# Kernel tuning notes

Hardware: AMD Instinct MI355X
Metric: run time of the kernel (lower is better)

Reference implementation:

```python
import jax, jax.numpy as jnp
import numpy as np

B, T, D = 256, 128, 64
H, A, O = 512, 128, 32


def setup_inputs() -> dict:
    key = jax.random.key(0)
    ks = jax.random.split(key, 16)
    u = lambda k, sh, lo, hi: jax.random.uniform(k, sh, jnp.float32, lo, hi)
    return {
        "x_states": jax.random.normal(ks[0], (B, T, D), jnp.float32),
        "x_dts": jax.random.uniform(ks[1], (B, T), jnp.float32) * 0.1,
        # StepwiseAttention params (stored [in, out])
        "Wq": u(ks[2], (D, A), -0.1, 0.1), "bq": u(ks[3], (A,), -0.1, 0.1),
        "Wk": u(ks[4], (H, A), -0.1, 0.1), "bk": u(ks[5], (A,), -0.1, 0.1),
        "Wv": u(ks[6], (H, A), -0.1, 0.1), "bv": u(ks[7], (A,), -0.1, 0.1),
        # LTCAttentionCell params
        "W_gd": u(ks[8], (D + H + A, 2 * H), -0.1, 0.1),
        "b_gd": u(ks[9], (2 * H,), -0.1, 0.1),
        "W_tau": u(ks[10], (H, H), -0.1, 0.1),
        "b_tau": u(ks[11], (H,), -0.1, 0.1),
        "gleak": u(ks[12], (H,), 0.001, 1.0),
        "cm": u(ks[13], (H,), 0.4, 0.6),
        # output head
        "W_fc": u(ks[14], (H, O), -0.1, 0.1),
        "b_fc": u(ks[15], (O,), -0.1, 0.1),
    }


def _forward(x_states, x_dts, Wq, bq, Wk, bk, Wv, bv,
             W_gd, b_gd, W_tau, b_tau, gleak, cm, W_fc, b_fc):
    scale = jnp.sqrt(jnp.asarray(A, jnp.float32))
    leak = jax.nn.softplus(cm) + jax.nn.softplus(gleak)  # [H]

    def dhdt(h, x_t, ctx):
        combined = jnp.concatenate([x_t, h, ctx], axis=1)        # [B, D+H+A]
        gd = combined @ W_gd + b_gd                              # [B, 2H]
        gate, dyn = jnp.split(gd, 2, axis=1)
        tau = jax.nn.softplus(h @ W_tau + b_tau)                 # [B, H]
        num = jax.nn.sigmoid(gate) * jnp.tanh(dyn) - h
        return num / (tau + leak + 1e-6)

    def step(carry, inp):
        h, hist = carry            # h [B,H], hist [B,T,H]
        t, x_t, dt = inp           # t scalar, x_t [B,D], dt [B]
        # stepwise attention over history h_1..h_t
        Q = x_t @ Wq + bq                                        # [B, A]
        K = hist @ Wk + bk                                       # [B, T, A]
        V = hist @ Wv + bv                                       # [B, T, A]
        scores = jnp.einsum('ba,bta->bt', Q, K) / scale          # [B, T]
        valid = jnp.arange(T) < t
        scores = jnp.where(valid[None, :], scores, -1e9)
        w = jax.nn.softmax(scores, axis=-1)
        ctx = jnp.einsum('bt,bta->ba', w, V)
        ctx = jnp.where(t > 0, ctx, jnp.zeros_like(ctx))         # empty history -> 0
        # one RK4 step (torchdiffeq 'rk4' = 3/8-rule variant), step size dt per sample
        dtc = dt[:, None]
        k1 = dhdt(h, x_t, ctx)
        k2 = dhdt(h + dtc * k1 / 3.0, x_t, ctx)
        k3 = dhdt(h + dtc * (k2 - k1 / 3.0), x_t, ctx)
        k4 = dhdt(h + dtc * (k1 - k2 + k3), x_t, ctx)
        h_next = h + dtc * (k1 + 3.0 * k2 + 3.0 * k3 + k4) / 8.0
        hist = jax.lax.dynamic_update_slice(hist, h_next[:, None, :], (0, t, 0))
        return (h_next, hist), None

    h0 = jnp.zeros((B, H), jnp.float32)
    hist0 = jnp.zeros((B, T, H), jnp.float32)
    xs = (jnp.arange(T), jnp.swapaxes(x_states, 0, 1), jnp.swapaxes(x_dts, 0, 1))
    (h_final, _), _ = jax.lax.scan(step, (h0, hist0), xs)
    return h_final @ W_fc + b_fc                                 # [B, O]


def reference(x_states, x_dts, Wq, bq, Wk, bk, Wv, bv,
              W_gd, b_gd, W_tau, b_tau, gleak, cm, W_fc, b_fc):
    return _forward(x_states, x_dts, Wq, bq, Wk, bk, Wv, bv,
                    W_gd, b_gd, W_tau, b_tau, gleak, cm, W_fc, b_fc)
```

## Files before the change

kernel.cpp:

```cpp
#include <hip/hip_runtime.h>
#include <math.h>

#define B_ 256
#define T_ 128
#define D_ 64
#define H_ 512
#define A_ 128
#define O_ 32

typedef __attribute__((ext_vector_type(8))) short short8;
typedef __attribute__((ext_vector_type(8))) unsigned short ushort8;
typedef __attribute__((ext_vector_type(4))) float floatx4;
typedef __attribute__((ext_vector_type(4))) unsigned int uintx4;
typedef unsigned long long ull;

__device__ __forceinline__ float sp_(float x) {
    return fmaxf(x, 0.f) + log1pf(expf(-fabsf(x)));
}
__device__ __forceinline__ float sigm_(float x) {
    return 1.f / (1.f + expf(-x));
}
__device__ __forceinline__ unsigned short f2bf_(float f) {
    unsigned int u = __float_as_uint(f);
    return (unsigned short)((u + 0x7FFFu + ((u >> 16) & 1u)) >> 16);
}
__device__ __forceinline__ float bf2f_(unsigned short u) {
    return __uint_as_float(((unsigned)u) << 16);
}

__device__ __forceinline__ void ld16sc(uintx4& d, const void* p) {
    asm volatile("global_load_dwordx4 %0, %1, off sc0 sc1"
                 : "=v"(d) : "v"(p) : "memory");
}
__device__ __forceinline__ void ld4sc(float& d, const void* p) {
    asm volatile("global_load_dword %0, %1, off sc0 sc1"
                 : "=v"(d) : "v"(p) : "memory");
}
__device__ __forceinline__ void ld4su(unsigned& d, const void* p) {
    asm volatile("global_load_dword %0, %1, off sc0 sc1"
                 : "=v"(d) : "v"(p) : "memory");
}
__device__ __forceinline__ void st64sc(ull* p, ull v) {
    asm volatile("global_store_dwordx2 %0, %1, off sc0 sc1"
                 :: "v"(p), "v"(v) : "memory");
}
__device__ __forceinline__ void stu32sc(unsigned* p, unsigned v) {
    asm volatile("global_store_dword %0, %1, off sc0 sc1"
                 :: "v"(p), "v"(v) : "memory");
}
__device__ __forceinline__ void vmwait4(uintx4& a, uintx4& b, uintx4& c,
                                        uintx4& d) {
    asm volatile("s_waitcnt vmcnt(0)"
                 : "+v"(a), "+v"(b), "+v"(c), "+v"(d)::"memory");
}
__device__ __forceinline__ void vmwait8(uintx4& a, uintx4& b, uintx4& c,
                                        uintx4& d, uintx4& e, uintx4& f,
                                        uintx4& g, uintx4& h) {
    asm volatile("s_waitcnt vmcnt(0)"
                 : "+v"(a), "+v"(b), "+v"(c), "+v"(d), "+v"(e), "+v"(f),
                   "+v"(g), "+v"(h)::"memory");
}
__device__ __forceinline__ void vmwait16f(float& a0, float& a1, float& a2,
                                          float& a3, float& a4, float& a5,
                                          float& a6, float& a7, float& b0,
                                          float& b1, float& b2, float& b3,
                                          float& b4, float& b5, float& b6,
                                          float& b7) {
    asm volatile("s_waitcnt vmcnt(0)"
                 : "+v"(a0), "+v"(a1), "+v"(a2), "+v"(a3), "+v"(a4), "+v"(a5),
                   "+v"(a6), "+v"(a7), "+v"(b0), "+v"(b1), "+v"(b2), "+v"(b3),
                   "+v"(b4), "+v"(b5), "+v"(b6), "+v"(b7)::"memory");
}
__device__ __forceinline__ void vmwait8u(unsigned& a, unsigned& b, unsigned& c,
                                         unsigned& d, unsigned& e, unsigned& f,
                                         unsigned& g, unsigned& h) {
    asm volatile("s_waitcnt vmcnt(0)"
                 : "+v"(a), "+v"(b), "+v"(c), "+v"(d), "+v"(e), "+v"(f),
                   "+v"(g), "+v"(h)::"memory");
}
__device__ __forceinline__ void vmwait4u(unsigned& a, unsigned& b, unsigned& c,
                                         unsigned& d) {
    asm volatile("s_waitcnt vmcnt(0)"
                 : "+v"(a), "+v"(b), "+v"(c), "+v"(d)::"memory");
}
__device__ __forceinline__ void vmwait1u(unsigned& a) {
    asm volatile("s_waitcnt vmcnt(0)" : "+v"(a)::"memory");
}
__device__ __forceinline__ floatx4 u2f_(uintx4 u) {
    union { uintx4 u; floatx4 f; } c;
    c.u = u;
    return c.f;
}
__device__ __forceinline__ void stf_(float* p, float v) {
    __hip_atomic_store(p, v, __ATOMIC_RELAXED, __HIP_MEMORY_SCOPE_SYSTEM);
}

__global__ void init_kernel(unsigned short* __restrict__ hpack,
                            unsigned* __restrict__ bar) {
    int i = blockIdx.x * 256 + threadIdx.x;
    if (i < B_ * H_) hpack[i] = 0;
    if (i < 18432) bar[i] = 0u;
}

__global__ void pack_w_kernel(const float* __restrict__ W_gd,
                              const float* __restrict__ W_tau,
                              const float* __restrict__ Wk,
                              const float* __restrict__ Wv,
                              unsigned short* __restrict__ Wpack) {
    int gid = blockIdx.x * 256 + threadIdx.x;
    if (gid >= 1114112) return;
    int j = gid & 7;
    int l = (gid >> 3) & 63;
    int kpart = (l >> 4) * 8 + j;
    int npart = l & 15;
    float v;
    if (gid < 786432) {
        int f = gid >> 9;
        int s = f % 3;
        int rem = f / 3;
        int kb = rem & 15, ct = rem >> 4;
        int k = kb * 32 + kpart;
        int c = ct * 16 + npart;
        if (s == 0)      v = W_gd[(size_t)(D_ + k) * 1024 + c];
        else if (s == 1) v = W_gd[(size_t)(D_ + k) * 1024 + 512 + c];
        else             v = W_tau[(size_t)k * 512 + c];
    } else if (gid < 851968) {
        int r = gid - 786432;
        int f = r >> 9;
        int s = f & 1, kb = (f >> 1) & 1, ct = f >> 2;
        int k = kb * 32 + kpart;
        int c = ct * 16 + npart;
        v = W_gd[(size_t)k * 1024 + s * 512 + c];
    } else if (gid < 983040) {
        int r = gid - 851968;
        int f = r >> 9;
        int s = f & 1, kb = (f >> 1) & 3, ct = f >> 3;
        int k = kb * 32 + kpart;
        int c = ct * 16 + npart;
        v = W_gd[(size_t)(D_ + H_ + k) * 1024 + s * 512 + c];
    } else {
        int r = gid - 983040;
        int f = r >> 9;
        int kb = f & 15, c4 = f >> 4;
        int k = kb * 32 + kpart;
        int n = (c4 & 7) * 16 + npart;
        v = (c4 < 8) ? Wk[(size_t)k * A_ + n] : Wv[(size_t)k * A_ + n];
    }
    Wpack[gid] = f2bf_(v);
}

__device__ __forceinline__ void gsyncF(unsigned* flags, int j, unsigned cnt) {
    asm volatile("s_waitcnt vmcnt(0)" ::: "memory");
    __syncthreads();
    if (threadIdx.x == 0) stu32sc(flags + j * 64, cnt);
    if (threadIdx.x < 8) {
        unsigned v;
        do {
            ld4su(v, flags + threadIdx.x * 64);
            vmwait1u(v);
            if (v >= cnt) break;
            __builtin_amdgcn_s_sleep(1);
        } while (true);
    }
    __syncthreads();
}

struct P {
    const float *x, *dts, *Wq, *bq, *bk, *bv, *b_gd, *b_tau, *gleak, *cm,
        *W_fc, *b_fc;
    float *h, *ctx, *out, *Kpart, *Vpart;
    unsigned short* Kh;
    const unsigned short *Wy, *Wx, *Wc, *Wkv;
    unsigned short *hpack, *yapack, *ybpack, *ycpack;
    unsigned* bar;
};

__global__ __launch_bounds__(256, 1) void fused_kernel(P p) {
    const int tid = threadIdx.x;
    const int bid = blockIdx.x;
    const int lane = tid & 63;
    const int wave = tid >> 6;
    const int g = bid & 15;
    const int j = bid >> 4;
    const int ct = j * 4 + wave;
    unsigned* flags = p.bar + g * 512;
    unsigned* senbase = p.bar + 8192;
    #define SEN(kind, src) (senbase + (((kind)*16 + g) * 8 + (src)) * 16)

    __shared__ float WqL[D_ * 129];
    __shared__ float xs4[2][D_];
    __shared__ float q4[2][A_];
    __shared__ float sc4[2][T_];
    __shared__ float red[2][2];
    __shared__ __align__(16) unsigned short AsL[32 * 256];
    __shared__ __align__(16) unsigned short ypbuf[4 * 256];
    __shared__ __align__(16) unsigned short As2[2 * 512];
    __shared__ unsigned short VhL[2][A_][136];

    const int quad = lane >> 4;
    const int c = ct * 16 + (lane & 15);
    const float btau = p.b_tau[c];
    const float lk = sp_(p.cm[c]) + sp_(p.gleak[c]) + 1e-6f;
    const float bgd_g = p.b_gd[c];
    const float bgd_d = p.b_gd[512 + c];
    const int aoff = (quad >> 1) * 256 + (lane & 15) * 16 + (quad & 1) * 8;
    const int ypw = wave * 256 + (lane & 15);

    const int sub = tid >> 7;
    const int tl = tid & 127;
    const int r = g * 16 + j * 2 + sub;
    const int rrow = r & 15;

    short8 wg[16], wd[16], wt[16];
    short8 wxg[2], wxd[2], wcg[4], wcd[4];
    {
        const short8* Wy8 = (const short8*)p.Wy;
        #pragma unroll
        for (int kb = 0; kb < 16; ++kb) {
            wg[kb] = Wy8[((ct * 16 + kb) * 3 + 0) * 64 + lane];
            wd[kb] = Wy8[((ct * 16 + kb) * 3 + 1) * 64 + lane];
            wt[kb] = Wy8[((ct * 16 + kb) * 3 + 2) * 64 + lane];
        }
        const short8* Wx8 = (const short8*)p.Wx;
        const short8* Wc8 = (const short8*)p.Wc;
        #pragma unroll
        for (int kb = 0; kb < 2; ++kb) {
            wxg[kb] = Wx8[((ct * 2 + kb) * 2 + 0) * 64 + lane];
            wxd[kb] = Wx8[((ct * 2 + kb) * 2 + 1) * 64 + lane];
        }
        #pragma unroll
        for (int kb = 0; kb < 4; ++kb) {
            wcg[kb] = Wc8[((ct * 4 + kb) * 2 + 0) * 64 + lane];
            wcd[kb] = Wc8[((ct * 4 + kb) * 2 + 1) * 64 + lane];
        }
    }

    for (int i = tid; i < D_ * A_; i += 256) {
        int d = i >> 7, a = i & 127;
        WqL[d * 129 + a] = p.Wq[i];
    }

    floatx4 hreg = {0.f, 0.f, 0.f, 0.f};
    floatx4 rk1, rk2, rk3, baseg, based, ycur, dt4;

    const short8* Wkv8 = (const short8*)p.Wkv;

    __syncthreads();

    for (int t = 0; t < T_; ++t) {
        {
            float kk[8], vv[8];
            uintx4 av[4];
            {
                const unsigned short* src = p.hpack + g * 8192;
                const unsigned expv = (unsigned)t;
                unsigned s0, s1, s2, s3, s4, s5, s6, s7;
                for (;;) {
                    #pragma unroll
                    for (int jj = 0; jj < 8; ++jj) {
                        ld4sc(kk[jj],
                              p.Kpart + ((g * 8 + jj) * 16 + rrow) * 128 + tl);
                        ld4sc(vv[jj],
                              p.Vpart + ((g * 8 + jj) * 16 + rrow) * 128 + tl);
                    }
                    #pragma unroll
                    for (int i = 0; i < 4; ++i)
                        ld16sc(av[i], src + (size_t)tid * 8 + i * 2048);
                    ld4su(s0, SEN(4, 0)); ld4su(s1, SEN(4, 1));
                    ld4su(s2, SEN(4, 2)); ld4su(s3, SEN(4, 3));
                    ld4su(s4, SEN(4, 4)); ld4su(s5, SEN(4, 5));
                    ld4su(s6, SEN(4, 6)); ld4su(s7, SEN(4, 7));
                    vmwait16f(kk[0], kk[1], kk[2], kk[3], kk[4], kk[5], kk[6],
                              kk[7], vv[0], vv[1], vv[2], vv[3], vv[4], vv[5],
                              vv[6], vv[7]);
                    vmwait4(av[0], av[1], av[2], av[3]);
                    vmwait8u(s0, s1, s2, s3, s4, s5, s6, s7);
                    if (s0 >= expv && s1 >= expv && s2 >= expv && s3 >= expv &&
                        s4 >= expv && s5 >= expv && s6 >= expv && s7 >= expv)
                        break;
                    __builtin_amdgcn_s_sleep(1);
                }
            }
            #pragma unroll
            for (int i = 0; i < 4; ++i)
                ((uintx4*)AsL)[tid + i * 256] = av[i];
            if (t > 0) {
                float ks = p.bk[tl], vs = p.bv[tl];
                #pragma unroll
                for (int jj = 0; jj < 8; ++jj) {
                    ks += kk[jj];
                    vs += vv[jj];
                }
                p.Kh[(size_t)(r * T_ + (t - 1)) * A_ + tl] = f2bf_(ks);
                VhL[sub][tl][t - 1] = f2bf_(vs);
            }
            if (tl < 16)
                ((float4*)xs4[sub])[tl] =
                    ((const float4*)&p.x[(r * T_ + t) * D_])[tl];
            __syncthreads();
            float qa = p.bq[tl];
            #pragma unroll 8
            for (int d = 0; d < D_; ++d) qa += xs4[sub][d] * WqL[d * 129 + tl];
            q4[sub][tl] = qa;
            __syncthreads();
            if (t == 0) {
                stf_(p.ctx + r * A_ + tl, 0.f);
            } else {
                const float rscale = 0.08838834764831845f;
                const int grp = tl >> 4, ln = tl & 15;
                float qv[8];
                #pragma unroll
                for (int i = 0; i < 8; ++i) qv[i] = q4[sub][ln * 8 + i];
                for (int s = grp; s < t; s += 8) {
                    ushort8 k8 = *((const ushort8*)(p.Kh +
                                     (size_t)(r * T_ + s) * A_) + ln);
                    float a2 = 0.f;
                    #pragma unroll
                    for (int i = 0; i < 8; ++i) a2 += bf2f_(k8[i]) * qv[i];
                    #pragma unroll
                    for (int off = 8; off > 0; off >>= 1)
                        a2 += __shfl_xor(a2, off, 16);
                    if (ln == 0) sc4[sub][s] = a2 * rscale;
                }
                __syncthreads();
                float mloc = -1e30f;
                for (int s = tl; s < t; s += 128) mloc = fmaxf(mloc, sc4[sub][s]);
                #pragma unroll
                for (int off = 32; off > 0; off >>= 1)
                    mloc = fmaxf(mloc, __shfl_xor(mloc, off, 64));
                if (lane == 0) red[sub][wave & 1] = mloc;
                __syncthreads();
                float m = fmaxf(red[sub][0], red[sub][1]);
                float ssum = 0.f;
                for (int s = tl; s < t; s += 128) {
                    float e = expf(sc4[sub][s] - m);
                    sc4[sub][s] = e;
                    ssum += e;
                }
                #pragma unroll
                for (int off = 32; off > 0; off >>= 1)
                    ssum += __shfl_xor(ssum, off, 64);
                __syncthreads();
                if (lane == 0) red[sub][wave & 1] = ssum;
                __syncthreads();
                float rs = 1.f / (red[sub][0] + red[sub][1]);
                const unsigned short* Vrow = &VhL[sub][tl][0];
                float ca0 = 0.f, ca1 = 0.f;
                int s0 = 0;
                for (; s0 + 16 <= t; s0 += 16) {
                    ushort8 v0 = *(const ushort8*)(Vrow + s0);
                    ushort8 v1 = *(const ushort8*)(Vrow + s0 + 8);
                    #pragma unroll
                    for (int i = 0; i < 8; ++i) {
                        ca0 += sc4[sub][s0 + i] * bf2f_(v0[i]);
                        ca1 += sc4[sub][s0 + 8 + i] * bf2f_(v1[i]);
                    }
                }
                if (s0 + 8 <= t) {
                    ushort8 v0 = *(const ushort8*)(Vrow + s0);
                    #pragma unroll
                    for (int i = 0; i < 8; ++i)
                        ca0 += sc4[sub][s0 + i] * bf2f_(v0[i]);
                    s0 += 8;
                }
                for (; s0 < t; ++s0) ca0 += sc4[sub][s0] * bf2f_(Vrow[s0]);
                stf_(p.ctx + r * A_ + tl, (ca0 + ca1) * rs);
            }
        }
        asm volatile("s_waitcnt vmcnt(0)" ::: "memory");
        __syncthreads();
        if (tid == 0) stu32sc(SEN(0, j), (unsigned)(t + 1));

        {
            const int mrow = lane & 15;
            const float* crow = &p.ctx[(g * 16 + mrow) * A_];
            uintx4 cc[8];
            {
                const unsigned* senp = SEN(0, mrow >> 1);
                const unsigned expv = (unsigned)(t + 1);
                unsigned sv;
                for (;;) {
                    #pragma unroll
                    for (int kb = 0; kb < 4; ++kb) {
                        ld16sc(cc[2 * kb], crow + kb * 32 + quad * 8);
                        ld16sc(cc[2 * kb + 1], crow + kb * 32 + quad * 8 + 4);
                    }
                    ld4su(sv, senp);
                    vmwait8(cc[0], cc[1], cc[2], cc[3], cc[4], cc[5], cc[6],
                            cc[7]);
                    vmwait1u(sv);
                    if (sv >= expv) break;
                    __builtin_amdgcn_s_sleep(1);
                }
            }
            #pragma unroll
            for (int i = 0; i < 4; ++i)
                dt4[i] = p.dts[(g * 16 + quad * 4 + i) * T_ + t];

            floatx4 bg = {0.f, 0.f, 0.f, 0.f};
            floatx4 bd = {0.f, 0.f, 0.f, 0.f};
            const float4* xrow =
                (const float4*)&p.x[((g * 16 + mrow) * T_ + t) * D_];
            #pragma unroll
            for (int kb = 0; kb < 2; ++kb) {
                float4 u = xrow[kb * 8 + quad * 2], v = xrow[kb * 8 + quad * 2 + 1];
                short8 ax;
                ax[0] = (short)f2bf_(u.x); ax[1] = (short)f2bf_(u.y);
                ax[2] = (short)f2bf_(u.z); ax[3] = (short)f2bf_(u.w);
                ax[4] = (short)f2bf_(v.x); ax[5] = (short)f2bf_(v.y);
                ax[6] = (short)f2bf_(v.z); ax[7] = (short)f2bf_(v.w);
                bg = __builtin_amdgcn_mfma_f32_16x16x32_bf16(ax, wxg[kb], bg, 0, 0, 0);
                bd = __builtin_amdgcn_mfma_f32_16x16x32_bf16(ax, wxd[kb], bd, 0, 0, 0);
            }
            #pragma unroll
            for (int kb = 0; kb < 4; ++kb) {
                floatx4 f0 = u2f_(cc[2 * kb]), f1 = u2f_(cc[2 * kb + 1]);
                short8 ac;
                ac[0] = (short)f2bf_(f0[0]); ac[1] = (short)f2bf_(f0[1]);
                ac[2] = (short)f2bf_(f0[2]); ac[3] = (short)f2bf_(f0[3]);
                ac[4] = (short)f2bf_(f1[0]); ac[5] = (short)f2bf_(f1[1]);
                ac[6] = (short)f2bf_(f1[2]); ac[7] = (short)f2bf_(f1[3]);
                bg = __builtin_amdgcn_mfma_f32_16x16x32_bf16(ac, wcg[kb], bg, 0, 0, 0);
                bd = __builtin_amdgcn_mfma_f32_16x16x32_bf16(ac, wcd[kb], bd, 0, 0, 0);
            }
            floatx4 ag = {0.f, 0.f, 0.f, 0.f};
            floatx4 ad = {0.f, 0.f, 0.f, 0.f};
            floatx4 at = {0.f, 0.f, 0.f, 0.f};
            #pragma unroll
            for (int kb = 0; kb < 16; ++kb) {
                short8 a = *(const short8*)(AsL + kb * 512 + aoff);
                ag = __builtin_amdgcn_mfma_f32_16x16x32_bf16(a, wg[kb], ag, 0, 0, 0);
                ad = __builtin_amdgcn_mfma_f32_16x16x32_bf16(a, wd[kb], ad, 0, 0, 0);
                at = __builtin_amdgcn_mfma_f32_16x16x32_bf16(a, wt[kb], at, 0, 0, 0);
            }
            #pragma unroll
            for (int i = 0; i < 4; ++i) {
                baseg[i] = bg[i] + bgd_g;
                based[i] = bd[i] + bgd_d;
                float gate = ag[i] + baseg[i];
                float dyn = ad[i] + based[i];
                float tau = sp_(at[i] + btau);
                float ki = (sigm_(gate) * tanhf(dyn) - hreg[i]) / (tau + lk);
                rk1[i] = ki;
                float yn = hreg[i] + dt4[i] * ki * (1.f / 3.f);
                ycur[i] = yn;
                ypbuf[ypw + (quad * 4 + i) * 16] = f2bf_(yn);
            }
            __syncthreads();
            st64sc((ull*)p.yapack + g * 2048 + j * 256 + tid,
                   ((const ull*)ypbuf)[tid]);
        }
        asm volatile("s_waitcnt vmcnt(0)" ::: "memory");
        __syncthreads();
        if (tid == 0) stu32sc(SEN(1, j), (unsigned)(t + 1));

        #pragma unroll 1
        for (int stage = 2; stage <= 4; ++stage) {
            const unsigned short* ysrc =
                (stage == 2) ? p.yapack : (stage == 3) ? p.ybpack : p.ycpack;
            unsigned short* ydst =
                (stage == 2) ? p.ybpack : (stage == 3) ? p.ycpack : p.hpack;
            const int senk = stage - 1;
            {
                const unsigned short* src = ysrc + g * 8192;
                const unsigned expv = (unsigned)(t + 1);
                const int sb = tid >> 7;
                uintx4 av[4];
                unsigned s0, s1, s2, s3;
                for (;;) {
                    #pragma unroll
                    for (int i = 0; i < 4; ++i)
                        ld16sc(av[i], src + (size_t)tid * 8 + i * 2048);
                    ld4su(s0, SEN(senk, sb + 0));
                    ld4su(s1, SEN(senk, sb + 2));
                    ld4su(s2, SEN(senk, sb + 4));
                    ld4su(s3, SEN(senk, sb + 6));
                    vmwait4(av[0], av[1], av[2], av[3]);
                    vmwait4u(s0, s1, s2, s3);
                    if (s0 >= expv && s1 >= expv && s2 >= expv && s3 >= expv)
                        break;
                    __builtin_amdgcn_s_sleep(1);
                }
                #pragma unroll
                for (int i = 0; i < 4; ++i)
                    ((uintx4*)AsL)[tid + i * 256] = av[i];
            }
            __syncthreads();
            floatx4 ag = {0.f, 0.f, 0.f, 0.f};
            floatx4 ad = {0.f, 0.f, 0.f, 0.f};
            floatx4 at = {0.f, 0.f, 0.f, 0.f};
            #pragma unroll
            for (int kb = 0; kb < 16; ++kb) {
                short8 a = *(const short8*)(AsL + kb * 512 + aoff);
                ag = __builtin_amdgcn_mfma_f32_16x16x32_bf16(a, wg[kb], ag, 0, 0, 0);
                ad = __builtin_amdgcn_mfma_f32_16x16x32_bf16(a, wd[kb], ad, 0, 0, 0);
                at = __builtin_amdgcn_mfma_f32_16x16x32_bf16(a, wt[kb], at, 0, 0, 0);
            }
            const int lane_p = ((c >> 3) & 3) * 16;
            #pragma unroll
            for (int i = 0; i < 4; ++i) {
                float gate = ag[i] + baseg[i];
                float dyn = ad[i] + based[i];
                float tau = sp_(at[i] + btau);
                float ki = (sigm_(gate) * tanhf(dyn) - ycur[i]) / (tau + lk);
                float yn;
                if (stage == 2) {
                    rk2[i] = ki;
                    yn = hreg[i] + dt4[i] * (ki - rk1[i] * (1.f / 3.f));
                } else if (stage == 3) {
                    rk3[i] = ki;
                    yn = hreg[i] + dt4[i] * (rk1[i] - rk2[i] + ki);
                } else {
                    yn = hreg[i] +
                         dt4[i] * (rk1[i] + 3.f * rk2[i] + 3.f * rk3[i] + ki) * 0.125f;
                    hreg[i] = yn;
                }
                ycur[i] = yn;
                ypbuf[ypw + (quad * 4 + i) * 16] = f2bf_(yn);
                if (stage == 4)
                    As2[(wave >> 1) * 512 + (c & 7) +
                        (lane_p + quad * 4 + i) * 8] = f2bf_(yn);
            }
            __syncthreads();
            st64sc((ull*)ydst + g * 2048 + j * 256 + tid,
                   ((const ull*)ypbuf)[tid]);
            if (stage == 4) {
                #pragma unroll
                for (int h4 = 0; h4 < 4; ++h4) {
                    const int c4 = wave + h4 * 4;
                    floatx4 acc = {0.f, 0.f, 0.f, 0.f};
                    #pragma unroll
                    for (int kk2 = 0; kk2 < 2; ++kk2) {
                        short8 a = *(const short8*)(As2 + (kk2 * 64 + lane) * 8);
                        acc = __builtin_amdgcn_mfma_f32_16x16x32_bf16(
                            a, Wkv8[(c4 * 16 + (j * 2 + kk2)) * 64 + lane], acc,
                            0, 0, 0);
                    }
                    const int ac = (c4 & 7) * 16 + (lane & 15);
                    float* part = (c4 < 8) ? p.Kpart : p.Vpart;
                    #pragma unroll
                    for (int i = 0; i < 4; ++i)
                        stf_(part + ((g * 8 + j) * 16 + quad * 4 + i) * 128 + ac,
                             acc[i]);
                }
            }
            asm volatile("s_waitcnt vmcnt(0)" ::: "memory");
            __syncthreads();
            if (tid == 0) stu32sc(SEN(stage, j), (unsigned)(t + 1));
        }
    }

    #pragma unroll
    for (int i = 0; i < 4; ++i)
        stf_(p.h + (g * 16 + quad * 4 + i) * H_ + c, hreg[i]);
    gsyncF(flags, j, 1u);
    {
        const int o = tl & 31, ks = tl >> 5;
        float acc = 0.f;
        const float* hrow = p.h + r * H_ + ks * 128;
        const float* wcol = p.W_fc + ks * 128 * O_ + o;
        #pragma unroll 1
        for (int rd = 0; rd < 4; ++rd) {
            uintx4 hh[8];
            #pragma unroll
            for (int i = 0; i < 8; ++i)
                ld16sc(hh[i], hrow + rd * 32 + i * 4);
            vmwait8(hh[0], hh[1], hh[2], hh[3], hh[4], hh[5], hh[6], hh[7]);
            #pragma unroll
            for (int i = 0; i < 8; ++i) {
                floatx4 f = u2f_(hh[i]);
                #pragma unroll
                for (int e = 0; e < 4; ++e)
                    acc += f[e] * wcol[(rd * 32 + i * 4 + e) * O_];
            }
        }
        sc4[sub][tl] = acc;
        __syncthreads();
        if (ks == 0)
            p.out[r * O_ + o] = acc + sc4[sub][o + 32] + sc4[sub][o + 64] +
                                sc4[sub][o + 96] + p.b_fc[o];
    }
    #undef SEN
}

extern "C" void kernel_launch(void* const* d_in, const int* in_sizes, int n_in,
                              void* d_out, int out_size, void* d_ws,
                              size_t ws_size, hipStream_t stream) {
    (void)in_sizes; (void)n_in; (void)out_size; (void)ws_size;
    P p;
    p.x = (const float*)d_in[0];
    p.dts = (const float*)d_in[1];
    p.Wq = (const float*)d_in[2];
    p.bq = (const float*)d_in[3];
    const float* Wk = (const float*)d_in[4];
    p.bk = (const float*)d_in[5];
    const float* Wv = (const float*)d_in[6];
    p.bv = (const float*)d_in[7];
    const float* W_gd = (const float*)d_in[8];
    p.b_gd = (const float*)d_in[9];
    const float* W_tau = (const float*)d_in[10];
    p.b_tau = (const float*)d_in[11];
    p.gleak = (const float*)d_in[12];
    p.cm = (const float*)d_in[13];
    p.W_fc = (const float*)d_in[14];
    p.b_fc = (const float*)d_in[15];
    p.out = (float*)d_out;

    float* ws = (float*)d_ws;
    p.h = ws;
    p.ctx = p.h + B_ * H_;
    p.Kpart = p.ctx + B_ * A_;
    p.Vpart = p.Kpart + 262144;
    unsigned short* Wpack = (unsigned short*)(p.Vpart + 262144);
    p.Wy = Wpack;
    p.Wx = Wpack + 786432;
    p.Wc = Wpack + 851968;
    p.Wkv = Wpack + 983040;
    p.hpack = Wpack + 1114112;
    p.yapack = p.hpack + B_ * H_;
    p.ybpack = p.yapack + B_ * H_;
    p.ycpack = p.ybpack + B_ * H_;
    p.Kh = p.ycpack + B_ * H_;
    p.bar = (unsigned*)(p.Kh + (size_t)B_ * T_ * A_);

    init_kernel<<<512, 256, 0, stream>>>(p.hpack, p.bar);
    pack_w_kernel<<<4352, 256, 0, stream>>>(W_gd, W_tau, Wk, Wv, Wpack);

    fused_kernel<<<dim3(128), dim3(256), 0, stream>>>(p);
}
```

Baseline: 3.529 ms.

## Precompute partial attention over older history during stage 4, merge newest entry online

The attention over history h_1..h_{t-1} for step t+1 is now computed right after stage 4 of step t, using known keys, and stored as unnormalized numerator, denominator and max. At the start of the next step only the newest key/value row (K/V projection of h_t via MFMA over the full hidden vector) is computed locally and merged with an online-softmax update. This removes the separate ctx barrier/flag and the Kpart/Vpart cross-block reduction from the critical path. In exchange each block redoes the full 512-wide K/V projection for 16 rows and adds more LDS buffers.

```diff
diff --git a/kernel.cpp b/kernel.cpp
--- a/kernel.cpp
+++ b/kernel.cpp
@@ -32,10 +32,6 @@
     asm volatile("global_load_dwordx4 %0, %1, off sc0 sc1"
                  : "=v"(d) : "v"(p) : "memory");
 }
-__device__ __forceinline__ void ld4sc(float& d, const void* p) {
-    asm volatile("global_load_dword %0, %1, off sc0 sc1"
-                 : "=v"(d) : "v"(p) : "memory");
-}
 __device__ __forceinline__ void ld4su(unsigned& d, const void* p) {
     asm volatile("global_load_dword %0, %1, off sc0 sc1"
                  : "=v"(d) : "v"(p) : "memory");
@@ -60,16 +56,9 @@
                  : "+v"(a), "+v"(b), "+v"(c), "+v"(d), "+v"(e), "+v"(f),
                    "+v"(g), "+v"(h)::"memory");
 }
-__device__ __forceinline__ void vmwait16f(float& a0, float& a1, float& a2,
-                                          float& a3, float& a4, float& a5,
-                                          float& a6, float& a7, float& b0,
-                                          float& b1, float& b2, float& b3,
-                                          float& b4, float& b5, float& b6,
-                                          float& b7) {
+__device__ __forceinline__ void vmwait3c(uintx4& a, uintx4& b, uintx4& c) {
     asm volatile("s_waitcnt vmcnt(0)"
-                 : "+v"(a0), "+v"(a1), "+v"(a2), "+v"(a3), "+v"(a4), "+v"(a5),
-                   "+v"(a6), "+v"(a7), "+v"(b0), "+v"(b1), "+v"(b2), "+v"(b3),
-                   "+v"(b4), "+v"(b5), "+v"(b6), "+v"(b7)::"memory");
+                 : "+v"(a), "+v"(b), "+v"(c)::"memory");
 }
 __device__ __forceinline__ void vmwait8u(unsigned& a, unsigned& b, unsigned& c,
                                          unsigned& d, unsigned& e, unsigned& f,
@@ -168,7 +157,7 @@
 struct P {
     const float *x, *dts, *Wq, *bq, *bk, *bv, *b_gd, *b_tau, *gleak, *cm,
         *W_fc, *b_fc;
-    float *h, *ctx, *out, *Kpart, *Vpart;
+    float *h, *ctxB, *out;
     unsigned short* Kh;
     const unsigned short *Wy, *Wx, *Wc, *Wkv;
     unsigned short *hpack, *yapack, *ybpack, *ycpack;
@@ -194,8 +183,10 @@
     __shared__ float red[2][2];
     __shared__ __align__(16) unsigned short AsL[32 * 256];
     __shared__ __align__(16) unsigned short ypbuf[4 * 256];
-    __shared__ __align__(16) unsigned short As2[2 * 512];
     __shared__ unsigned short VhL[2][A_][136];
+    __shared__ __align__(16) float xsLf[16][68];
+    __shared__ __align__(16) unsigned short KVt[2][16][136];
+    __shared__ __align__(16) float ctxL[16][132];
 
     const int quad = lane >> 4;
     const int c = ct * 16 + (lane & 15);
@@ -209,7 +200,9 @@
     const int sub = tid >> 7;
     const int tl = tid & 127;
     const int r = g * 16 + j * 2 + sub;
-    const int rrow = r & 15;
+    const int row16 = tid >> 4;
+    const int k16 = tid & 15;
+    const float rscale = 0.08838834764831845f;
 
     short8 wg[16], wd[16], wt[16];
     short8 wxg[2], wxd[2], wcg[4], wcd[4];
@@ -248,155 +241,114 @@
     __syncthreads();
 
     for (int t = 0; t < T_; ++t) {
+        uintx4 cb0 = {0, 0, 0, 0}, cb1 = {0, 0, 0, 0}, cbs = {0, 0, 0, 0};
         {
-            float kk[8], vv[8];
             uintx4 av[4];
-            {
-                const unsigned short* src = p.hpack + g * 8192;
-                const unsigned expv = (unsigned)t;
-                unsigned s0, s1, s2, s3, s4, s5, s6, s7;
-                for (;;) {
-                    #pragma unroll
-                    for (int jj = 0; jj < 8; ++jj) {
-                        ld4sc(kk[jj],
-                              p.Kpart + ((g * 8 + jj) * 16 + rrow) * 128 + tl);
-                        ld4sc(vv[jj],
-                              p.Vpart + ((g * 8 + jj) * 16 + rrow) * 128 + tl);
-                    }
-                    #pragma unroll
-                    for (int i = 0; i < 4; ++i)
-                        ld16sc(av[i], src + (size_t)tid * 8 + i * 2048);
-                    ld4su(s0, SEN(4, 0)); ld4su(s1, SEN(4, 1));
-                    ld4su(s2, SEN(4, 2)); ld4su(s3, SEN(4, 3));
-                    ld4su(s4, SEN(4, 4)); ld4su(s5, SEN(4, 5));
-                    ld4su(s6, SEN(4, 6)); ld4su(s7, SEN(4, 7));
-                    vmwait16f(kk[0], kk[1], kk[2], kk[3], kk[4], kk[5], kk[6],
-                              kk[7], vv[0], vv[1], vv[2], vv[3], vv[4], vv[5],
-                              vv[6], vv[7]);
-                    vmwait4(av[0], av[1], av[2], av[3]);
-                    vmwait8u(s0, s1, s2, s3, s4, s5, s6, s7);
-                    if (s0 >= expv && s1 >= expv && s2 >= expv && s3 >= expv &&
-                        s4 >= expv && s5 >= expv && s6 >= expv && s7 >= expv)
-                        break;
-                    __builtin_amdgcn_s_sleep(1);
+            const unsigned short* srcp = p.hpack + g * 8192;
+            const float* cbrow = p.ctxB + (size_t)(g * 16 + row16) * 132;
+            const unsigned expv = (unsigned)t;
+            unsigned s0, s1, s2, s3, s4, s5, s6, s7;
+            for (;;) {
+                #pragma unroll
+                for (int i = 0; i < 4; ++i)
+                    ld16sc(av[i], srcp + (size_t)tid * 8 + i * 2048);
+                if (t > 0) {
+                    ld16sc(cb0, cbrow + k16 * 8);
+                    ld16sc(cb1, cbrow + k16 * 8 + 4);
+                    ld16sc(cbs, cbrow + 128);
                 }
+                ld4su(s0, SEN(4, 0)); ld4su(s1, SEN(4, 1));
+                ld4su(s2, SEN(4, 2)); ld4su(s3, SEN(4, 3));
+                ld4su(s4, SEN(4, 4)); ld4su(s5, SEN(4, 5));
+                ld4su(s6, SEN(4, 6)); ld4su(s7, SEN(4, 7));
+                vmwait4(av[0], av[1], av[2], av[3]);
+                if (t > 0) vmwait3c(cb0, cb1, cbs);
+                vmwait8u(s0, s1, s2, s3, s4, s5, s6, s7);
+                if (s0 >= expv && s1 >= expv && s2 >= expv && s3 >= expv &&
+                    s4 >= expv && s5 >= expv && s6 >= expv && s7 >= expv)
+                    break;
+                __builtin_amdgcn_s_sleep(1);
             }
             #pragma unroll
             for (int i = 0; i < 4; ++i)
                 ((uintx4*)AsL)[tid + i * 256] = av[i];
-            if (t > 0) {
-                float ks = p.bk[tl], vs = p.bv[tl];
-                #pragma unroll
-                for (int jj = 0; jj < 8; ++jj) {
-                    ks += kk[jj];
-                    vs += vv[jj];
+            if (t > 0 && tid < 64)
+                ((float4*)&xsLf[tid >> 2][0])[tid & 3] =
+                    ((const float4*)&p.x[((g * 16 + (tid >> 2)) * T_ + t) *
+                                         D_])[tid & 3];
+        }
+        __syncthreads();
+
+        if (t > 0) {
+            #pragma unroll
+            for (int h4 = 0; h4 < 4; ++h4) {
+                const int c4 = wave + h4 * 4;
+                floatx4 acc = {0.f, 0.f, 0.f, 0.f};
+                #pragma unroll
+                for (int kb = 0; kb < 16; ++kb) {
+                    short8 a = *(const short8*)(AsL + kb * 512 + aoff);
+                    acc = __builtin_amdgcn_mfma_f32_16x16x32_bf16(
+                        a, Wkv8[(c4 * 16 + kb) * 64 + lane], acc, 0, 0, 0);
                 }
-                p.Kh[(size_t)(r * T_ + (t - 1)) * A_ + tl] = f2bf_(ks);
-                VhL[sub][tl][t - 1] = f2bf_(vs);
-            }
-            if (tl < 16)
-                ((float4*)xs4[sub])[tl] =
-                    ((const float4*)&p.x[(r * T_ + t) * D_])[tl];
+                const int ac = (c4 & 7) * 16 + (lane & 15);
+                const float bias = ((c4 < 8) ? p.bk : p.bv)[ac];
+                #pragma unroll
+                for (int i = 0; i < 4; ++i)
+                    KVt[c4 >= 8 ? 1 : 0][quad * 4 + i][ac] =
+                        f2bf_(acc[i] + bias);
+            }
             __syncthreads();
-            float qa = p.bq[tl];
-            #pragma unroll 8
-            for (int d = 0; d < D_; ++d) qa += xs4[sub][d] * WqL[d * 129 + tl];
-            q4[sub][tl] = qa;
+            {
+                float qa[8];
+                #pragma unroll
+                for (int n = 0; n < 8; ++n) qa[n] = p.bq[k16 * 8 + n];
+                for (int d = 0; d < D_; ++d) {
+                    float xv = xsLf[row16][d];
+                    #pragma unroll
+                    for (int n = 0; n < 8; ++n)
+                        qa[n] += xv * WqL[d * 129 + k16 * 8 + n];
+                }
+                ushort8 k8 = *(const ushort8*)&KVt[0][row16][k16 * 8];
+                float sm = 0.f;
+                #pragma unroll
+                for (int n = 0; n < 8; ++n) sm += qa[n] * bf2f_(k8[n]);
+                #pragma unroll
+                for (int off = 8; off > 0; off >>= 1)
+                    sm += __shfl_xor(sm, off, 16);
+                sm *= rscale;
+                floatx4 cbf = u2f_(cbs);
+                const float denb = cbf[0], mb = cbf[1];
+                const float m = fmaxf(mb, sm);
+                const float wb = expf(mb - m), wm = expf(sm - m);
+                const float rs = 1.f / (denb * wb + wm);
+                floatx4 n0 = u2f_(cb0), n1 = u2f_(cb1);
+                ushort8 v8 = *(const ushort8*)&KVt[1][row16][k16 * 8];
+                #pragma unroll
+                for (int n = 0; n < 4; ++n)
+                    ctxL[row16][k16 * 8 + n] =
+                        (n0[n] * wb + wm * bf2f_(v8[n])) * rs;
+                #pragma unroll
+                for (int n = 0; n < 4; ++n)
+                    ctxL[row16][k16 * 8 + 4 + n] =
+                        (n1[n] * wb + wm * bf2f_(v8[4 + n])) * rs;
+            }
             __syncthreads();
-            if (t == 0) {
-                stf_(p.ctx + r * A_ + tl, 0.f);
-            } else {
-                const float rscale = 0.08838834764831845f;
-                const int grp = tl >> 4, ln = tl & 15;
-                float qv[8];
-                #pragma unroll
-                for (int i = 0; i < 8; ++i) qv[i] = q4[sub][ln * 8 + i];
-                for (int s = grp; s < t; s += 8) {
-                    ushort8 k8 = *((const ushort8*)(p.Kh +
-                                     (size_t)(r * T_ + s) * A_) + ln);
-                    float a2 = 0.f;
-                    #pragma unroll
-                    for (int i = 0; i < 8; ++i) a2 += bf2f_(k8[i]) * qv[i];
-                    #pragma unroll
-                    for (int off = 8; off > 0; off >>= 1)
-                        a2 += __shfl_xor(a2, off, 16);
-                    if (ln == 0) sc4[sub][s] = a2 * rscale;
-                }
-                __syncthreads();
-                float mloc = -1e30f;
-                for (int s = tl; s < t; s += 128) mloc = fmaxf(mloc, sc4[sub][s]);
-                #pragma unroll
-                for (int off = 32; off > 0; off >>= 1)
-                    mloc = fmaxf(mloc, __shfl_xor(mloc, off, 64));
-                if (lane == 0) red[sub][wave & 1] = mloc;
-                __syncthreads();
-                float m = fmaxf(red[sub][0], red[sub][1]);
-                float ssum = 0.f;
-                for (int s = tl; s < t; s += 128) {
-                    float e = expf(sc4[sub][s] - m);
-                    sc4[sub][s] = e;
-                    ssum += e;
-                }
-                #pragma unroll
-                for (int off = 32; off > 0; off >>= 1)
-                    ssum += __shfl_xor(ssum, off, 64);
-                __syncthreads();
-                if (lane == 0) red[sub][wave & 1] = ssum;
-                __syncthreads();
-                float rs = 1.f / (red[sub][0] + red[sub][1]);
-                const unsigned short* Vrow = &VhL[sub][tl][0];
-                float ca0 = 0.f, ca1 = 0.f;
-                int s0 = 0;
-                for (; s0 + 16 <= t; s0 += 16) {
-                    ushort8 v0 = *(const ushort8*)(Vrow + s0);
-                    ushort8 v1 = *(const ushort8*)(Vrow + s0 + 8);
-                    #pragma unroll
-                    for (int i = 0; i < 8; ++i) {
-                        ca0 += sc4[sub][s0 + i] * bf2f_(v0[i]);
-                        ca1 += sc4[sub][s0 + 8 + i] * bf2f_(v1[i]);
-                    }
-                }
-                if (s0 + 8 <= t) {
-                    ushort8 v0 = *(const ushort8*)(Vrow + s0);
-                    #pragma unroll
-                    for (int i = 0; i < 8; ++i)
-                        ca0 += sc4[sub][s0 + i] * bf2f_(v0[i]);
-                    s0 += 8;
-                }
-                for (; s0 < t; ++s0) ca0 += sc4[sub][s0] * bf2f_(Vrow[s0]);
-                stf_(p.ctx + r * A_ + tl, (ca0 + ca1) * rs);
-            }
-        }
-        asm volatile("s_waitcnt vmcnt(0)" ::: "memory");
-        __syncthreads();
-        if (tid == 0) stu32sc(SEN(0, j), (unsigned)(t + 1));
+            {
+                const int rl = j * 2 + sub;
+                p.Kh[(size_t)(r * T_ + (t - 1)) * A_ + tl] = KVt[0][rl][tl];
+                VhL[sub][tl][t - 1] = KVt[1][rl][tl];
+            }
+        } else {
+            #pragma unroll
+            for (int n = 0; n < 8; ++n) ctxL[row16][k16 * 8 + n] = 0.f;
+            __syncthreads();
+        }
 
         {
-            const int mrow = lane & 15;
-            const float* crow = &p.ctx[(g * 16 + mrow) * A_];
-            uintx4 cc[8];
-            {
-                const unsigned* senp = SEN(0, mrow >> 1);
-                const unsigned expv = (unsigned)(t + 1);
-                unsigned sv;
-                for (;;) {
-                    #pragma unroll
-                    for (int kb = 0; kb < 4; ++kb) {
-                        ld16sc(cc[2 * kb], crow + kb * 32 + quad * 8);
-                        ld16sc(cc[2 * kb + 1], crow + kb * 32 + quad * 8 + 4);
-                    }
-                    ld4su(sv, senp);
-                    vmwait8(cc[0], cc[1], cc[2], cc[3], cc[4], cc[5], cc[6],
-                            cc[7]);
-                    vmwait1u(sv);
-                    if (sv >= expv) break;
-                    __builtin_amdgcn_s_sleep(1);
-                }
-            }
             #pragma unroll
             for (int i = 0; i < 4; ++i)
                 dt4[i] = p.dts[(g * 16 + quad * 4 + i) * T_ + t];
-
+            const int mrow = lane & 15;
             floatx4 bg = {0.f, 0.f, 0.f, 0.f};
             floatx4 bd = {0.f, 0.f, 0.f, 0.f};
             const float4* xrow =
@@ -414,12 +366,13 @@
             }
             #pragma unroll
             for (int kb = 0; kb < 4; ++kb) {
-                floatx4 f0 = u2f_(cc[2 * kb]), f1 = u2f_(cc[2 * kb + 1]);
+                float4 f0 = *(const float4*)&ctxL[mrow][kb * 32 + quad * 8];
+                float4 f1 = *(const float4*)&ctxL[mrow][kb * 32 + quad * 8 + 4];
                 short8 ac;
-                ac[0] = (short)f2bf_(f0[0]); ac[1] = (short)f2bf_(f0[1]);
-                ac[2] = (short)f2bf_(f0[2]); ac[3] = (short)f2bf_(f0[3]);
-                ac[4] = (short)f2bf_(f1[0]); ac[5] = (short)f2bf_(f1[1]);
-                ac[6] = (short)f2bf_(f1[2]); ac[7] = (short)f2bf_(f1[3]);
+                ac[0] = (short)f2bf_(f0.x); ac[1] = (short)f2bf_(f0.y);
+                ac[2] = (short)f2bf_(f0.z); ac[3] = (short)f2bf_(f0.w);
+                ac[4] = (short)f2bf_(f1.x); ac[5] = (short)f2bf_(f1.y);
+                ac[6] = (short)f2bf_(f1.z); ac[7] = (short)f2bf_(f1.w);
                 bg = __builtin_amdgcn_mfma_f32_16x16x32_bf16(ac, wcg[kb], bg, 0, 0, 0);
                 bd = __builtin_amdgcn_mfma_f32_16x16x32_bf16(ac, wcd[kb], bd, 0, 0, 0);
             }
@@ -496,7 +449,6 @@
                 ad = __builtin_amdgcn_mfma_f32_16x16x32_bf16(a, wd[kb], ad, 0, 0, 0);
                 at = __builtin_amdgcn_mfma_f32_16x16x32_bf16(a, wt[kb], at, 0, 0, 0);
             }
-            const int lane_p = ((c >> 3) & 3) * 16;
             #pragma unroll
             for (int i = 0; i < 4; ++i) {
                 float gate = ag[i] + baseg[i];
@@ -517,31 +469,88 @@
                 }
                 ycur[i] = yn;
                 ypbuf[ypw + (quad * 4 + i) * 16] = f2bf_(yn);
-                if (stage == 4)
-                    As2[(wave >> 1) * 512 + (c & 7) +
-                        (lane_p + quad * 4 + i) * 8] = f2bf_(yn);
             }
             __syncthreads();
             st64sc((ull*)ydst + g * 2048 + j * 256 + tid,
                    ((const ull*)ypbuf)[tid]);
-            if (stage == 4) {
-                #pragma unroll
-                for (int h4 = 0; h4 < 4; ++h4) {
-                    const int c4 = wave + h4 * 4;
-                    floatx4 acc = {0.f, 0.f, 0.f, 0.f};
+
+            if (stage == 4 && t + 1 < T_) {
+                float num = 0.f, den = 0.f, m = -1e30f;
+                if (t > 0) {
+                    if (tl < 16)
+                        ((float4*)xs4[sub])[tl] =
+                            ((const float4*)&p.x[(r * T_ + (t + 1)) * D_])[tl];
+                    __syncthreads();
+                    float qa = p.bq[tl];
+                    #pragma unroll 8
+                    for (int d = 0; d < D_; ++d)
+                        qa += xs4[sub][d] * WqL[d * 129 + tl];
+                    q4[sub][tl] = qa;
+                    __syncthreads();
+                    const int grp = tl >> 4, ln = tl & 15;
+                    float qv[8];
                     #pragma unroll
-                    for (int kk2 = 0; kk2 < 2; ++kk2) {
-                        short8 a = *(const short8*)(As2 + (kk2 * 64 + lane) * 8);
-                        acc = __builtin_amdgcn_mfma_f32_16x16x32_bf16(
-                            a, Wkv8[(c4 * 16 + (j * 2 + kk2)) * 64 + lane], acc,
-                            0, 0, 0);
+                    for (int i = 0; i < 8; ++i) qv[i] = q4[sub][ln * 8 + i];
+                    for (int s = grp; s < t; s += 8) {
+                        ushort8 k8 = *((const ushort8*)(p.Kh +
+                                         (size_t)(r * T_ + s) * A_) + ln);
+                        float a2 = 0.f;
+                        #pragma unroll
+                        for (int i = 0; i < 8; ++i) a2 += bf2f_(k8[i]) * qv[i];
+                        #pragma unroll
+                        for (int off = 8; off > 0; off >>= 1)
+                            a2 += __shfl_xor(a2, off, 16);
+                        if (ln == 0) sc4[sub][s] = a2 * rscale;
                     }
-                    const int ac = (c4 & 7) * 16 + (lane & 15);
-                    float* part = (c4 < 8) ? p.Kpart : p.Vpart;
+                    __syncthreads();
+                    float mloc = -1e30f;
+                    for (int s = tl; s < t; s += 128)
+                        mloc = fmaxf(mloc, sc4[sub][s]);
                     #pragma unroll
-                    for (int i = 0; i < 4; ++i)
-                        stf_(part + ((g * 8 + j) * 16 + quad * 4 + i) * 128 + ac,
-                             acc[i]);
+                    for (int off = 32; off > 0; off >>= 1)
+                        mloc = fmaxf(mloc, __shfl_xor(mloc, off, 64));
+                    if (lane == 0) red[sub][wave & 1] = mloc;
+                    __syncthreads();
+                    m = fmaxf(red[sub][0], red[sub][1]);
+                    float ssum = 0.f;
+                    for (int s = tl; s < t; s += 128) {
+                        float e = expf(sc4[sub][s] - m);
+                        sc4[sub][s] = e;
+                        ssum += e;
+                    }
+                    #pragma unroll
+                    for (int off = 32; off > 0; off >>= 1)
+                        ssum += __shfl_xor(ssum, off, 64);
+                    __syncthreads();
+                    if (lane == 0) red[sub][wave & 1] = ssum;
+                    __syncthreads();
+                    den = red[sub][0] + red[sub][1];
+                    const unsigned short* Vrow = &VhL[sub][tl][0];
+                    float ca0 = 0.f, ca1 = 0.f;
+                    int s0 = 0;
+                    for (; s0 + 16 <= t; s0 += 16) {
+                        ushort8 v0 = *(const ushort8*)(Vrow + s0);
+                        ushort8 v1 = *(const ushort8*)(Vrow + s0 + 8);
+                        #pragma unroll
+                        for (int i = 0; i < 8; ++i) {
+                            ca0 += sc4[sub][s0 + i] * bf2f_(v0[i]);
+                            ca1 += sc4[sub][s0 + 8 + i] * bf2f_(v1[i]);
+                        }
+                    }
+                    if (s0 + 8 <= t) {
+                        ushort8 v0 = *(const ushort8*)(Vrow + s0);
+                        #pragma unroll
+                        for (int i = 0; i < 8; ++i)
+                            ca0 += sc4[sub][s0 + i] * bf2f_(v0[i]);
+                        s0 += 8;
+                    }
+                    for (; s0 < t; ++s0) ca0 += sc4[sub][s0] * bf2f_(Vrow[s0]);
+                    num = ca0 + ca1;
+                }
+                stf_(p.ctxB + (size_t)r * 132 + tl, num);
+                if (tl == 0) {
+                    stf_(p.ctxB + (size_t)r * 132 + 128, den);
+                    stf_(p.ctxB + (size_t)r * 132 + 129, m);
                 }
             }
             asm volatile("s_waitcnt vmcnt(0)" ::: "memory");
@@ -608,10 +617,8 @@
 
     float* ws = (float*)d_ws;
     p.h = ws;
-    p.ctx = p.h + B_ * H_;
-    p.Kpart = p.ctx + B_ * A_;
-    p.Vpart = p.Kpart + 262144;
-    unsigned short* Wpack = (unsigned short*)(p.Vpart + 262144);
+    p.ctxB = p.h + B_ * H_;
+    unsigned short* Wpack = (unsigned short*)(p.ctxB + B_ * 132);
     p.Wy = Wpack;
     p.Wx = Wpack + 786432;
     p.Wc = Wpack + 851968;
```

New measurement: 5.054 ms. 43.2% more time.
